# Optimization experiments

Measured on AMD Instinct MI355X. Metric: run time of the kernel, lower is better.

## Reference

```python
import jax, jax.numpy as jnp
import numpy as np

B, T, D, H, L, R, V = 4, 1024, 1024, 16, 12, 32, 50257
HD = D // H
SCALING = 2.0   # lora_alpha(64) / lora_rank(32) at the default 16-bit precision
EPS = 1e-5
KV_QMAX = float(2 ** 8 - 1)  # kv_cache_bits = 8 (middle of [4,8,16])


def _ln(x, g, b):
    m = jnp.mean(x, -1, keepdims=True)
    v = jnp.mean(jnp.square(x - m), -1, keepdims=True)
    return (x - m) * jax.lax.rsqrt(v + EPS) * g + b


def _round_ste(x):
    return x + jax.lax.stop_gradient(jnp.round(x) - x)


def _fake_quant(x, mn, mx):
    # asymmetric learnable fake-quant with straight-through rounding
    scale = (mx - mn) / KV_QMAX
    zp = _round_ste(-mn / scale)
    q = jnp.clip(_round_ste(x / scale) + zp, 0.0, KV_QMAX)
    return (q - zp) * scale


def _sp_linear(x, w, b, la, lb):
    # quantized-base linear (full precision at 16-bit) + LoRA adapter (eval: no dropout)
    return x @ w + b + SCALING * ((x @ la) @ lb)


def setup_inputs() -> dict:
    key = jax.random.key(0)
    ks = iter(jax.random.split(key, 64))
    rn = lambda shape, s=0.02: jax.random.normal(next(ks), shape, jnp.float32) * s
    return {
        "input_ids": jax.random.randint(next(ks), (B, T), 0, V),
        "wte": rn((V, D)), "wpe": rn((T, D)),
        "ln1_g": jnp.ones((L, D)), "ln1_b": jnp.zeros((L, D)),
        "attn_w": rn((L, D, 3 * D)), "attn_b": jnp.zeros((L, 3 * D)),
        "attn_la": rn((L, D, R)), "attn_lb": rn((L, R, 3 * D)),
        "proj_w": rn((L, D, D)), "proj_b": jnp.zeros((L, D)),
        "proj_la": rn((L, D, R)), "proj_lb": rn((L, R, D)),
        "ln2_g": jnp.ones((L, D)), "ln2_b": jnp.zeros((L, D)),
        "fc_w": rn((L, D, 4 * D)), "fc_b": jnp.zeros((L, 4 * D)),
        "fc_la": rn((L, D, R)), "fc_lb": rn((L, R, 4 * D)),
        "mproj_w": rn((L, 4 * D, D)), "mproj_b": jnp.zeros((L, D)),
        "mproj_la": rn((L, 4 * D, R)), "mproj_lb": rn((L, R, D)),
        "kv_min": jnp.full((L,), -4.0), "kv_max": jnp.full((L,), 4.0),
        "lnf_g": jnp.ones((D,)), "lnf_b": jnp.zeros((D,)),
    }


def reference(input_ids, wte, wpe, ln1_g, ln1_b, attn_w, attn_b, attn_la, attn_lb,
              proj_w, proj_b, proj_la, proj_lb, ln2_g, ln2_b, fc_w, fc_b, fc_la,
              fc_lb, mproj_w, mproj_b, mproj_la, mproj_lb, kv_min, kv_max,
              lnf_g, lnf_b):
    mask = jnp.tril(jnp.ones((T, T), bool))
    h = wte[input_ids] + wpe[None, :T]  # [B,T,D] (dropout is identity in eval)

    def block(h, p):
        (g1, b1, aw, ab, ala, alb, pw, pb, pla, plb, g2, b2,
         fw, fb, fla, flb, mw, mb, mla, mlb, mn, mx) = p
        x = _ln(h, g1, b1)
        qkv = _sp_linear(x, aw, ab, ala, alb)  # [B,T,3D]
        q, k, v = jnp.split(qkv, 3, axis=-1)
        heads = lambda t: t.reshape(B, T, H, HD).transpose(0, 2, 1, 3)  # bhtd
        q, k, v = heads(q), heads(k), heads(v)
        # KV-cache fake quantization (default precision flag unset on attn)
        k = _fake_quant(k, mn, mx)
        v = _fake_quant(v, mn, mx)
        att = jnp.einsum('bhqd,bhkd->bhqk', q, k) / np.float32(np.sqrt(HD))
        att = jax.nn.softmax(jnp.where(mask, att, -jnp.inf), axis=-1)
        o = jnp.einsum('bhqk,bhkd->bhqd', att, v).transpose(0, 2, 1, 3).reshape(B, T, D)
        h = h + _sp_linear(o, pw, pb, pla, plb)
        x = _ln(h, g2, b2)
        m = jax.nn.gelu(_sp_linear(x, fw, fb, fla, flb), approximate=False)
        h = h + _sp_linear(m, mw, mb, mla, mlb)
        return h, None

    params = (ln1_g, ln1_b, attn_w, attn_b, attn_la, attn_lb, proj_w, proj_b,
              proj_la, proj_lb, ln2_g, ln2_b, fc_w, fc_b, fc_la, fc_lb,
              mproj_w, mproj_b, mproj_la, mproj_lb, kv_min, kv_max)
    h, _ = jax.lax.scan(block, h, params)
    return _ln(h, lnf_g, lnf_b)
```

## Files before the change

### kernel.cpp

```cpp
#include <hip/hip_runtime.h>
#include <hip/hip_bf16.h>


typedef __bf16 bf16x8 __attribute__((ext_vector_type(8)));
typedef float f32x4 __attribute__((ext_vector_type(4)));

static __device__ __forceinline__ float bf2f(unsigned short u) {
    union { unsigned int i; float f; } c; c.i = ((unsigned int)u) << 16; return c.f;
}
static __device__ __forceinline__ unsigned short f2bf(float f) {
    unsigned int u = __float_as_uint(f);
    u += 0x7fffu + ((u >> 16) & 1u);
    return (unsigned short)(u >> 16);
}

#define GL2LDS(g, l) __builtin_amdgcn_global_load_lds( \
    (const __attribute__((address_space(1))) unsigned int*)(g), \
    (__attribute__((address_space(3))) unsigned int*)(l), 16, 0, 0)

__global__ __launch_bounds__(256) void k_embed(const int* __restrict__ ids,
        const float* __restrict__ wte, const float* __restrict__ wpe,
        float* __restrict__ h) {
    int row = blockIdx.x;
    int t = row & 1023;
    int id = ids[row];
    int d = threadIdx.x * 4;
    float4 a = *(const float4*)(wte + (size_t)id * 1024 + d);
    float4 b = *(const float4*)(wpe + (size_t)t * 1024 + d);
    float4 o = make_float4(a.x + b.x, a.y + b.y, a.z + b.z, a.w + b.w);
    *(float4*)(h + (size_t)row * 1024 + d) = o;
}

template <bool BF16OUT>
__global__ __launch_bounds__(256) void k_ln(const float* __restrict__ h,
        const float* __restrict__ g, const float* __restrict__ be,
        unsigned short* __restrict__ xo, float* __restrict__ fo) {
    int row = blockIdx.x, tid = threadIdx.x;
    float4 v = *(const float4*)(h + (size_t)row * 1024 + tid * 4);
    float s = v.x + v.y + v.z + v.w;
    for (int off = 32; off; off >>= 1) s += __shfl_down(s, off);
    __shared__ float red[8];
    int wid = tid >> 6, lane = tid & 63;
    if (!lane) red[wid] = s;
    __syncthreads();
    float mean = (red[0] + red[1] + red[2] + red[3]) * (1.f / 1024.f);
    float dx = v.x - mean, dy = v.y - mean, dz = v.z - mean, dw = v.w - mean;
    float q = dx * dx + dy * dy + dz * dz + dw * dw;
    for (int off = 32; off; off >>= 1) q += __shfl_down(q, off);
    if (!lane) red[4 + wid] = q;
    __syncthreads();
    float var = (red[4] + red[5] + red[6] + red[7]) * (1.f / 1024.f);
    float inv = 1.0f / sqrtf(var + 1e-5f);
    float4 gv = *(const float4*)(g + tid * 4);
    float4 bv = *(const float4*)(be + tid * 4);
    float y0 = dx * inv * gv.x + bv.x;
    float y1 = dy * inv * gv.y + bv.y;
    float y2 = dz * inv * gv.z + bv.z;
    float y3 = dw * inv * gv.w + bv.w;
    if (BF16OUT) {
        ushort4 o;
        o.x = f2bf(y0); o.y = f2bf(y1); o.z = f2bf(y2); o.w = f2bf(y3);
        *(ushort4*)(xo + (size_t)row * 1024 + tid * 4) = o;
    } else {
        *(float4*)(fo + (size_t)row * 1024 + tid * 4) = make_float4(y0, y1, y2, y3);
    }
}

__global__ __launch_bounds__(64) void k_lora_mfma(const unsigned short* __restrict__ A,
        const unsigned short* __restrict__ laT, unsigned short* __restrict__ tmp, int K) {
    int rowBase = blockIdx.x * 16;
    int lane = threadIdx.x;
    int lrow = lane & 15, lk8 = (lane >> 4) * 8;
    f32x4 acc0 = {0.f, 0.f, 0.f, 0.f}, acc1 = {0.f, 0.f, 0.f, 0.f};
    const unsigned short* arow = A + (size_t)(rowBase + lrow) * K + lk8;
    const unsigned short* b0p = laT + (size_t)lrow * K + lk8;
    const unsigned short* b1p = laT + (size_t)(16 + lrow) * K + lk8;
#pragma unroll 2
    for (int kt = 0; kt < K; kt += 32) {
        bf16x8 af = *(const bf16x8*)(arow + kt);
        bf16x8 b0 = *(const bf16x8*)(b0p + kt);
        bf16x8 b1 = *(const bf16x8*)(b1p + kt);
        acc0 = __builtin_amdgcn_mfma_f32_16x16x32_bf16(af, b0, acc0, 0, 0, 0);
        acc1 = __builtin_amdgcn_mfma_f32_16x16x32_bf16(af, b1, acc1, 0, 0, 0);
    }
    int lq = lane >> 4;
#pragma unroll
    for (int rg = 0; rg < 4; ++rg) {
        int row = rowBase + lq * 4 + rg;
        tmp[(size_t)row * 64 + lrow] = f2bf(acc0[rg]);
        tmp[(size_t)row * 64 + 16 + lrow] = f2bf(acc1[rg]);
        tmp[(size_t)row * 64 + 32 + lrow] = 0;
        tmp[(size_t)row * 64 + 48 + lrow] = 0;
    }
}

__global__ __launch_bounds__(256) void k_prep(
        const float* aw, const float* pw, const float* fw, const float* mw,
        const float* alb, const float* plb, const float* flb, const float* mlb,
        const float* ala, const float* pla, const float* fla, const float* mla,
        unsigned short* WTq, unsigned short* WTp, unsigned short* WTf, unsigned short* WTm,
        unsigned short* LTq, unsigned short* LTp, unsigned short* LTf, unsigned short* LTm,
        unsigned short* LAq, unsigned short* LAp, unsigned short* LAf, unsigned short* LAm) {
    int bid = blockIdx.x;
    const float* src; unsigned short* dst; int K, N, ntn, local, dstS; float scale = 1.f;
    if      (bid < 768)  { src = aw;  dst = WTq; K = 1024; N = 3072; ntn = 48; local = bid; dstS = K; }
    else if (bid < 1024) { src = pw;  dst = WTp; K = 1024; N = 1024; ntn = 16; local = bid - 768; dstS = K; }
    else if (bid < 2048) { src = fw;  dst = WTf; K = 1024; N = 4096; ntn = 64; local = bid - 1024; dstS = K; }
    else if (bid < 3072) { src = mw;  dst = WTm; K = 4096; N = 1024; ntn = 16; local = bid - 2048; dstS = K; }
    else if (bid < 3120) { src = alb; dst = LTq; K = 32;   N = 3072; ntn = 48; local = bid - 3072; scale = 2.f; dstS = 64; }
    else if (bid < 3136) { src = plb; dst = LTp; K = 32;   N = 1024; ntn = 16; local = bid - 3120; scale = 2.f; dstS = 64; }
    else if (bid < 3200) { src = flb; dst = LTf; K = 32;   N = 4096; ntn = 64; local = bid - 3136; scale = 2.f; dstS = 64; }
    else if (bid < 3216) { src = mlb; dst = LTm; K = 32;   N = 1024; ntn = 16; local = bid - 3200; scale = 2.f; dstS = 64; }
    else if (bid < 3232) { src = ala; dst = LAq; K = 1024; N = 32;   ntn = 1;  local = bid - 3216; dstS = K; }
    else if (bid < 3248) { src = pla; dst = LAp; K = 1024; N = 32;   ntn = 1;  local = bid - 3232; dstS = K; }
    else if (bid < 3264) { src = fla; dst = LAf; K = 1024; N = 32;   ntn = 1;  local = bid - 3248; dstS = K; }
    else                 { src = mla; dst = LAm; K = 4096; N = 32;   ntn = 1;  local = bid - 3264; dstS = K; }
    int kt = local / ntn, nt = local % ntn;
    int k0 = kt * 64, n0 = nt * 64;
    __shared__ unsigned short Tl[64][72];
    int tid = threadIdx.x;
    int cr = tid >> 6;
    int cc = tid & 63;
#pragma unroll
    for (int p = 0; p < 16; ++p) {
        int kl = p * 4 + cr;
        if (k0 + kl < K && n0 + cc < N) Tl[kl][cc] = f2bf(src[(size_t)(k0 + kl) * N + n0 + cc] * scale);
    }
    __syncthreads();
#pragma unroll
    for (int p = 0; p < 16; ++p) {
        int nl = p * 4 + cr;
        int kl = cc;
        if (n0 + nl < N) {
            if (k0 + kl < K) dst[(size_t)(n0 + nl) * dstS + k0 + kl] = Tl[kl][nl];
            else if (k0 + kl < dstS) dst[(size_t)(n0 + nl) * dstS + k0 + kl] = 0;
        }
    }
}

template <int EPI>
__global__ __launch_bounds__(256) void k_gemm(
        const unsigned short* __restrict__ A, const unsigned short* __restrict__ WT,
        const float* __restrict__ bias, const unsigned short* __restrict__ tmpA,
        const unsigned short* __restrict__ lbT, const float* __restrict__ res,
        float* __restrict__ outF, unsigned short* __restrict__ outH, int N, int K) {
    __shared__ unsigned short Al[128 * 32];
    __shared__ unsigned short Bl[128 * 32];
    int tid = threadIdx.x;
    int nBase = blockIdx.x * 128, rowBase = blockIdx.y * 128;
    int w = tid >> 6, lane = tid & 63;
    int wr = w >> 1, wc = w & 1;
    int lrow = lane & 15, lk8 = (lane >> 4) * 8;
    int srow = w * 32 + (lane >> 2);
    int scol = (lane & 3) * 8;
    f32x4 acc[4][4];
#pragma unroll
    for (int i = 0; i < 4; ++i)
#pragma unroll
        for (int j = 0; j < 4; ++j) acc[i][j] = f32x4{0.f, 0.f, 0.f, 0.f};
    int nk = K >> 5;
    for (int kt = 0; kt <= nk; ++kt) {
        bool mn = kt < nk;
        const unsigned short* sa0;
        const unsigned short* sa1;
        const unsigned short* sb0;
        const unsigned short* sb1;
        if (mn) {
            sa0 = A + (size_t)(rowBase + srow) * K + kt * 32 + scol;
            sa1 = A + (size_t)(rowBase + srow + 16) * K + kt * 32 + scol;
            sb0 = WT + (size_t)(nBase + srow) * K + kt * 32 + scol;
            sb1 = WT + (size_t)(nBase + srow + 16) * K + kt * 32 + scol;
        } else {
            sa0 = tmpA + (size_t)(rowBase + srow) * 64 + scol;
            sa1 = tmpA + (size_t)(rowBase + srow + 16) * 64 + scol;
            sb0 = lbT + (size_t)(nBase + srow) * 64 + scol;
            sb1 = lbT + (size_t)(nBase + srow + 16) * 64 + scol;
        }
        __syncthreads();
        GL2LDS(sa0, &Al[(w * 32) * 32]);
        GL2LDS(sa1, &Al[(w * 32 + 16) * 32]);
        GL2LDS(sb0, &Bl[(w * 32) * 32]);
        GL2LDS(sb1, &Bl[(w * 32 + 16) * 32]);
        __syncthreads();
        bf16x8 af[4], bfr[4];
#pragma unroll
        for (int mt = 0; mt < 4; ++mt) af[mt] = *(const bf16x8*)&Al[(wr * 64 + mt * 16 + lrow) * 32 + lk8];
#pragma unroll
        for (int nt = 0; nt < 4; ++nt) bfr[nt] = *(const bf16x8*)&Bl[(wc * 64 + nt * 16 + lrow) * 32 + lk8];
#pragma unroll
        for (int mt = 0; mt < 4; ++mt)
#pragma unroll
            for (int nt = 0; nt < 4; ++nt)
                acc[mt][nt] = __builtin_amdgcn_mfma_f32_16x16x32_bf16(af[mt], bfr[nt], acc[mt][nt], 0, 0, 0);
    }
    int lq = lane >> 4;
#pragma unroll
    for (int nt = 0; nt < 4; ++nt) {
        int col = nBase + wc * 64 + nt * 16 + lrow;
        float bv = bias[col];
#pragma unroll
        for (int mt = 0; mt < 4; ++mt) {
            int row0 = rowBase + wr * 64 + mt * 16 + lq * 4;
#pragma unroll
            for (int rg = 0; rg < 4; ++rg) {
                int row = row0 + rg;
                float v = acc[mt][nt][rg] + bv;
                size_t idx = (size_t)row * N + col;
                if (EPI == 1) v += res[idx];
                outF[idx] = v;
            }
        }
    }
}

template <int EPI>
__global__ __launch_bounds__(512, 1) void k_gemm256(
        const unsigned short* __restrict__ A, const unsigned short* __restrict__ WT,
        const float* __restrict__ bias, const unsigned short* __restrict__ tmpA,
        const unsigned short* __restrict__ lbT,
        const float* __restrict__ kvmin, const float* __restrict__ kvmax, int layer,
        unsigned short* __restrict__ qh, unsigned short* __restrict__ kh,
        unsigned short* __restrict__ vh,
        float* __restrict__ outF, unsigned short* __restrict__ outH, int N, int K) {
    __shared__ unsigned short lds[9 * 8192];
    const int tid = threadIdx.x;
    const int wid = tid >> 6, lane = tid & 63;
    const int wr = wid >> 2, wc = wid & 3;
    const int nBase = blockIdx.x * 256, rowBase = blockIdx.y * 256;
    const int nk = (K >> 6) + 1;

    f32x4 acc[8][4];
#pragma unroll
    for (int i = 0; i < 8; ++i)
#pragma unroll
        for (int j = 0; j < 4; ++j) acc[i][j] = f32x4{0.f, 0.f, 0.f, 0.f};

    auto stage = [&](int s) {
        int kt = s >> 2, part = s & 3;
        bool dead = kt >= nk;
        unsigned short* dst = &lds[(dead ? 8 : (s & 7)) * 8192];
        bool isA = part >= 2;
        int half = part & 1;
        bool lora = (kt == nk - 1);
#pragma unroll
        for (int i = 0; i < 2; ++i) {
            int o = ((i * 8 + wid) << 10) + (lane << 4);
            int r = o >> 7;
            int col = ((o & 127) ^ (((o >> 9) & 3) << 5)) >> 1;
            const unsigned short* src;
            if (dead) {
                src = A + (lane << 3);
            } else if (isA) {
                int grow = rowBase + half * 128 + r;
                src = lora ? tmpA + (size_t)grow * 64 + col
                           : A + (size_t)grow * K + kt * 64 + col;
            } else {
                int gcol = nBase + half * 128 + r;
                src = lora ? lbT + (size_t)gcol * 64 + col
                           : WT + (size_t)gcol * K + kt * 64 + col;
            }
            GL2LDS(src, dst + ((i * 8 + wid) << 9));
        }
    };

    stage(0); stage(1); stage(2); stage(3);
    stage(4); stage(5); stage(6);
    asm volatile("s_waitcnt vmcnt(6)" ::: "memory");
    __builtin_amdgcn_s_barrier();

    for (int kt = 0; kt < nk; ++kt) {
        const unsigned short* aPart = &lds[(((kt & 1) << 2) + 2 + wr) * 8192];
        const unsigned short* bPart = &lds[(((kt & 1) << 2) + (wc >> 1)) * 8192];
        bf16x8 bfr[4][2];
#pragma unroll
        for (int p = 0; p < 4; ++p) {
            bf16x8 af[2][2];
#pragma unroll
            for (int mm = 0; mm < 2; ++mm)
#pragma unroll
                for (int kk = 0; kk < 2; ++kk) {
                    int row = (p * 2 + mm) * 16 + (lane & 15);
                    int cb = (kk * 64 + ((lane >> 4) << 4)) ^ (((row >> 2) & 3) << 5);
                    af[mm][kk] = *(const bf16x8*)&aPart[row * 64 + (cb >> 1)];
                }
            if (p == 0) {
#pragma unroll
                for (int n = 0; n < 4; ++n)
#pragma unroll
                    for (int kk = 0; kk < 2; ++kk) {
                        int row = ((wc & 1) << 6) + n * 16 + (lane & 15);
                        int cb = (kk * 64 + ((lane >> 4) << 4)) ^ (((row >> 2) & 3) << 5);
                        bfr[n][kk] = *(const bf16x8*)&bPart[row * 64 + (cb >> 1)];
                    }
            }
            stage(p == 0 ? 4 * (kt + 1) + 3 : 4 * (kt + 2) + (p - 1));
            __builtin_amdgcn_s_barrier();
            __builtin_amdgcn_s_setprio(1);
#pragma unroll
            for (int mm = 0; mm < 2; ++mm)
#pragma unroll
                for (int n = 0; n < 4; ++n)
#pragma unroll
                    for (int kk = 0; kk < 2; ++kk)
                        acc[p * 2 + mm][n] = __builtin_amdgcn_mfma_f32_16x16x32_bf16(
                            af[mm][kk], bfr[n][kk], acc[p * 2 + mm][n], 0, 0, 0);
            __builtin_amdgcn_s_setprio(0);
            if (p == 3) asm volatile("s_waitcnt vmcnt(6)" ::: "memory");
            __builtin_amdgcn_s_barrier();
        }
    }

    if (EPI == 3) {
        const int b = rowBase >> 10, t0 = rowBase & 1023;
        const int sec = nBase >> 10, nb = nBase & 1023;
        const int lrow = lane & 15, lq4 = (lane >> 4) << 2;
        float qs = 1.f, qzp = 0.f, qinv = 1.f;
        if (sec) {
            float mnv = kvmin[layer], mxv = kvmax[layer];
            qs = (mxv - mnv) * (1.f / 255.f);
            qzp = rintf(-mnv / qs);
            qinv = 1.f / qs;
        }
#pragma unroll
        for (int n = 0; n < 4; ++n) {
            int dd = wc * 64 + n * 16 + lrow;
            float bv = bias[nBase + dd];
#pragma unroll
            for (int m = 0; m < 8; ++m) {
#pragma unroll
                for (int rg = 0; rg < 4; ++rg) {
                    int tt = wr * 128 + m * 16 + lq4 + rg;
                    float v = acc[m][n][rg] + bv;
                    if (sec) {
                        float qv = rintf(v * qinv) + qzp;
                        qv = fminf(fmaxf(qv, 0.f), 255.f);
                        v = (qv - qzp) * qs;
                    }
                    int r = (sec == 2) ? dd : tt;
                    int c = (sec == 2) ? tt : dd;
                    lds[r * 256 + (c ^ ((r & 7) << 3))] = f2bf(v);
                }
            }
        }
        __syncthreads();
        if (sec < 2) {
            unsigned short* dstp = sec ? kh : qh;
            int tL = tid & 255;
            int hp = tid >> 8;
#pragma unroll
            for (int hi = 0; hi < 2; ++hi) {
                int dL = (hp * 2 + hi) * 64;
                int hh = (nb >> 6) + hp * 2 + hi;
                size_t base = (((size_t)(b * 16 + hh)) * 1024 + t0 + tL) * 64;
#pragma unroll
                for (int j = 0; j < 8; ++j) {
                    int c = (dL + j * 8) ^ ((tL & 7) << 3);
                    *(uint4*)(dstp + base + j * 8) = *(const uint4*)&lds[tL * 256 + c];
                }
            }
        } else {
            int dL = tid & 255;
            int th = (tid >> 8) * 128;
            int hh = (nb >> 6) + (dL >> 6);
            size_t base = (((size_t)(b * 16 + hh)) * 64 + (dL & 63)) * 1024 + t0 + th;
#pragma unroll
            for (int j = 0; j < 16; ++j) {
                int c = (th + j * 8) ^ ((dL & 7) << 3);
                *(uint4*)(vh + base + j * 8) = *(const uint4*)&lds[dL * 256 + c];
            }
        }
    } else {
#pragma unroll
        for (int n = 0; n < 4; ++n) {
            int col = nBase + wc * 64 + n * 16 + (lane & 15);
            float bv = bias[col];
#pragma unroll
            for (int m = 0; m < 8; ++m) {
                int row0 = rowBase + wr * 128 + m * 16 + ((lane >> 4) << 2);
#pragma unroll
                for (int rg = 0; rg < 4; ++rg) {
                    int row = row0 + rg;
                    float v = acc[m][n][rg] + bv;
                    size_t idx = (size_t)row * N + col;
                    if (EPI == 2) {
                        v = 0.5f * v * (1.f + erff(v * 0.70710678118654752f));
                        outH[idx] = f2bf(v);
                    } else {
                        outF[idx] = v;
                    }
                }
            }
        }
    }
}

__global__ __launch_bounds__(256) void k_attn(const unsigned short* __restrict__ qh,
        const unsigned short* __restrict__ kh, const unsigned short* __restrict__ vh,
        unsigned short* __restrict__ o) {
    int fid = blockIdx.y * 16 + blockIdx.x;
    int wgid = (fid & 7) * 128 + (fid >> 3);
    int bh = wgid >> 4, qb = wgid & 15;
    int b = bh >> 4, hh = bh & 15;
    int tid = threadIdx.x, w = tid >> 6, lane = tid & 63;
    int cq = lane & 15;
    int g = lane >> 4;
    int lk8 = g * 8;
    __shared__ unsigned short Kl[64][72];
    __shared__ unsigned short Vt[64][72];
    __shared__ unsigned short Pl[4][16][72];
    const float SCL = 0.18033688011112042f;
    int qrow = qb * 64 + w * 16 + cq;
    bf16x8 aq[2];
    aq[0] = *(const bf16x8*)(qh + ((size_t)bh * 1024 + qrow) * 64 + lk8);
    aq[1] = *(const bf16x8*)(qh + ((size_t)bh * 1024 + qrow) * 64 + 32 + lk8);
    f32x4 od[4];
#pragma unroll
    for (int i = 0; i < 4; ++i) od[i] = f32x4{0.f, 0.f, 0.f, 0.f};
    float mrun = -3e38f, lrun = 0.f;
    int rl = tid >> 2, seg = (tid & 3) * 16;
    for (int kb = 0; kb <= qb; ++kb) {
        __syncthreads();
        {
            size_t kbase = ((size_t)bh * 1024 + kb * 64 + rl) * 64 + seg;
            *(uint4*)&Kl[rl][seg] = *(const uint4*)(kh + kbase);
            *(uint4*)&Kl[rl][seg + 8] = *(const uint4*)(kh + kbase + 8);
            size_t vbase = ((size_t)bh * 64 + rl) * 1024 + kb * 64 + seg;
            *(uint4*)&Vt[rl][seg] = *(const uint4*)(vh + vbase);
            *(uint4*)&Vt[rl][seg + 8] = *(const uint4*)(vh + vbase + 8);
        }
        __syncthreads();
        f32x4 st[4];
#pragma unroll
        for (int ktile = 0; ktile < 4; ++ktile) {
            f32x4 sacc = f32x4{0.f, 0.f, 0.f, 0.f};
#pragma unroll
            for (int dh = 0; dh < 2; ++dh) {
                bf16x8 bk = *(const bf16x8*)&Kl[ktile * 16 + cq][dh * 32 + lk8];
                sacc = __builtin_amdgcn_mfma_f32_16x16x32_bf16(bk, aq[dh], sacc, 0, 0, 0);
            }
            st[ktile] = sacc * SCL;
        }
        if (kb == qb) {
#pragma unroll
            for (int ktile = 0; ktile < 4; ++ktile) {
#pragma unroll
                for (int rg = 0; rg < 4; ++rg) {
                    int kidx = kb * 64 + ktile * 16 + g * 4 + rg;
                    if (kidx > qrow) st[ktile][rg] = -3e38f;
                }
            }
        }
        float pmax = st[0][0];
#pragma unroll
        for (int ktile = 0; ktile < 4; ++ktile)
#pragma unroll
            for (int rg = 0; rg < 4; ++rg) pmax = fmaxf(pmax, st[ktile][rg]);
        pmax = fmaxf(pmax, __shfl_xor(pmax, 16));
        pmax = fmaxf(pmax, __shfl_xor(pmax, 32));
        float mnew = fmaxf(mrun, pmax);
        float sum = 0.f;
#pragma unroll
        for (int ktile = 0; ktile < 4; ++ktile)
#pragma unroll
            for (int rg = 0; rg < 4; ++rg) {
                st[ktile][rg] = exp2f(st[ktile][rg] - mnew);
                sum += st[ktile][rg];
            }
        sum += __shfl_xor(sum, 16);
        sum += __shfl_xor(sum, 32);
        float corr = exp2f(mrun - mnew);
        lrun = lrun * corr + sum;
        mrun = mnew;
#pragma unroll
        for (int rg = 0; rg < 4; ++rg) {
            float cv = __shfl(corr, (lane & 48) | (g * 4 + rg));
#pragma unroll
            for (int dt = 0; dt < 4; ++dt) od[dt][rg] *= cv;
        }
#pragma unroll
        for (int ktile = 0; ktile < 4; ++ktile) {
            ushort4 pw;
            pw.x = f2bf(st[ktile][0]); pw.y = f2bf(st[ktile][1]);
            pw.z = f2bf(st[ktile][2]); pw.w = f2bf(st[ktile][3]);
            *(ushort4*)&Pl[w][cq][ktile * 16 + g * 4] = pw;
        }
        bf16x8 pa[2];
        pa[0] = *(const bf16x8*)&Pl[w][cq][lk8];
        pa[1] = *(const bf16x8*)&Pl[w][cq][32 + lk8];
#pragma unroll
        for (int dt = 0; dt < 4; ++dt) {
#pragma unroll
            for (int kh2 = 0; kh2 < 2; ++kh2) {
                bf16x8 bv = *(const bf16x8*)&Vt[dt * 16 + cq][kh2 * 32 + lk8];
                od[dt] = __builtin_amdgcn_mfma_f32_16x16x32_bf16(pa[kh2], bv, od[dt], 0, 0, 0);
            }
        }
    }
#pragma unroll
    for (int rg = 0; rg < 4; ++rg) {
        float lv = __shfl(lrun, (lane & 48) | (g * 4 + rg));
        float inv = 1.0f / lv;
        int row = qb * 64 + w * 16 + g * 4 + rg;
#pragma unroll
        for (int dt = 0; dt < 4; ++dt) {
            float val = od[dt][rg] * inv;
            o[((size_t)(b * 1024 + row)) * 1024 + hh * 64 + dt * 16 + cq] = f2bf(val);
        }
    }
}

extern "C" void kernel_launch(void* const* d_in, const int* in_sizes, int n_in,
                              void* d_out, int out_size, void* d_ws, size_t ws_size,
                              hipStream_t stream) {
    const int*   ids      = (const int*)d_in[0];
    const float* wte      = (const float*)d_in[1];
    const float* wpe      = (const float*)d_in[2];
    const float* ln1_g    = (const float*)d_in[3];
    const float* ln1_b    = (const float*)d_in[4];
    const float* attn_w   = (const float*)d_in[5];
    const float* attn_b   = (const float*)d_in[6];
    const float* attn_la  = (const float*)d_in[7];
    const float* attn_lb  = (const float*)d_in[8];
    const float* proj_w   = (const float*)d_in[9];
    const float* proj_b   = (const float*)d_in[10];
    const float* proj_la  = (const float*)d_in[11];
    const float* proj_lb  = (const float*)d_in[12];
    const float* ln2_g    = (const float*)d_in[13];
    const float* ln2_b    = (const float*)d_in[14];
    const float* fc_w     = (const float*)d_in[15];
    const float* fc_b     = (const float*)d_in[16];
    const float* fc_la    = (const float*)d_in[17];
    const float* fc_lb    = (const float*)d_in[18];
    const float* mproj_w  = (const float*)d_in[19];
    const float* mproj_b  = (const float*)d_in[20];
    const float* mproj_la = (const float*)d_in[21];
    const float* mproj_lb = (const float*)d_in[22];
    const float* kv_min   = (const float*)d_in[23];
    const float* kv_max   = (const float*)d_in[24];
    const float* lnf_g    = (const float*)d_in[25];
    const float* lnf_b    = (const float*)d_in[26];

    char* ws = (char*)d_ws;
    size_t off = 0;
    auto alloc = [&](size_t bytes) -> char* {
        char* p = ws + off;
        off = (off + bytes + 255) & ~(size_t)255;
        return p;
    };
    float*          h   = (float*)alloc(4096ull * 1024 * 4);
    unsigned short* xb  = (unsigned short*)alloc(4096ull * 1024 * 2);
    unsigned short* tmp = (unsigned short*)alloc(4096ull * 64 * 2);
    unsigned short* qhb = (unsigned short*)alloc(64ull * 1024 * 64 * 2);
    unsigned short* khb = (unsigned short*)alloc(64ull * 1024 * 64 * 2);
    unsigned short* vhb = (unsigned short*)alloc(64ull * 64 * 1024 * 2);
    unsigned short* ob  = (unsigned short*)alloc(4096ull * 1024 * 2);
    unsigned short* mb  = (unsigned short*)alloc(4096ull * 4096 * 2);
    unsigned short* WTq = (unsigned short*)alloc(3072ull * 1024 * 2);
    unsigned short* WTp = (unsigned short*)alloc(1024ull * 1024 * 2);
    unsigned short* WTf = (unsigned short*)alloc(4096ull * 1024 * 2);
    unsigned short* WTm = (unsigned short*)alloc(1024ull * 4096 * 2);
    unsigned short* LTq = (unsigned short*)alloc(3072ull * 64 * 2);
    unsigned short* LTp = (unsigned short*)alloc(1024ull * 64 * 2);
    unsigned short* LTf = (unsigned short*)alloc(4096ull * 64 * 2);
    unsigned short* LTm = (unsigned short*)alloc(1024ull * 64 * 2);
    unsigned short* LAq = (unsigned short*)alloc(32ull * 1024 * 2);
    unsigned short* LAp = (unsigned short*)alloc(32ull * 1024 * 2);
    unsigned short* LAf = (unsigned short*)alloc(32ull * 1024 * 2);
    unsigned short* LAm = (unsigned short*)alloc(32ull * 4096 * 2);

    k_embed<<<4096, 256, 0, stream>>>(ids, wte, wpe, h);
    for (int l = 0; l < 12; ++l) {
        k_prep<<<3328, 256, 0, stream>>>(
            attn_w + (size_t)l * 1024 * 3072, proj_w + (size_t)l * 1024 * 1024,
            fc_w + (size_t)l * 1024 * 4096, mproj_w + (size_t)l * 4096 * 1024,
            attn_lb + (size_t)l * 32 * 3072, proj_lb + (size_t)l * 32 * 1024,
            fc_lb + (size_t)l * 32 * 4096, mproj_lb + (size_t)l * 32 * 1024,
            attn_la + (size_t)l * 1024 * 32, proj_la + (size_t)l * 1024 * 32,
            fc_la + (size_t)l * 1024 * 32, mproj_la + (size_t)l * 4096 * 32,
            WTq, WTp, WTf, WTm, LTq, LTp, LTf, LTm, LAq, LAp, LAf, LAm);
        k_ln<true><<<4096, 256, 0, stream>>>(h, ln1_g + l * 1024, ln1_b + l * 1024, xb, nullptr);
        k_lora_mfma<<<256, 64, 0, stream>>>(xb, LAq, tmp, 1024);
        k_gemm256<3><<<dim3(12, 16), 512, 0, stream>>>(xb, WTq, attn_b + l * 3072, tmp, LTq,
                                                       kv_min, kv_max, l, qhb, khb, vhb,
                                                       nullptr, nullptr, 3072, 1024);
        k_attn<<<dim3(16, 64), 256, 0, stream>>>(qhb, khb, vhb, ob);
        k_lora_mfma<<<256, 64, 0, stream>>>(ob, LAp, tmp, 1024);
        k_gemm<1><<<dim3(8, 32), 256, 0, stream>>>(ob, WTp, proj_b + l * 1024, tmp, LTp,
                                                   h, h, nullptr, 1024, 1024);
        k_ln<true><<<4096, 256, 0, stream>>>(h, ln2_g + l * 1024, ln2_b + l * 1024, xb, nullptr);
        k_lora_mfma<<<256, 64, 0, stream>>>(xb, LAf, tmp, 1024);
        k_gemm256<2><<<dim3(16, 16), 512, 0, stream>>>(xb, WTf, fc_b + l * 4096, tmp, LTf,
                                                       nullptr, nullptr, 0, nullptr, nullptr, nullptr,
                                                       nullptr, mb, 4096, 1024);
        k_lora_mfma<<<256, 64, 0, stream>>>(mb, LAm, tmp, 4096);
        k_gemm<1><<<dim3(8, 32), 256, 0, stream>>>(mb, WTm, mproj_b + l * 1024, tmp, LTm,
                                                   h, h, nullptr, 1024, 4096);
    }
    k_ln<false><<<4096, 256, 0, stream>>>(h, lnf_g, lnf_b, nullptr, (float*)d_out);
}
```

Measured before the change: 4.419 ms.

## Split LoRA-A reduction across four waves and use 128x64 tiles for N=1024 GEMMs

The LoRA down-projection kernel now uses four waves per block. Each wave reduces a quarter of K, and the partial sums are combined through shared memory, so each block runs a quarter of the serial K loop. The proj and mproj GEMMs (N=1024) switch from 128x128 tiles with 4 waves to 128x64 tiles with 2 waves. This doubles the grid to 512 blocks for better CU occupancy on the wide GPU. The cost is more reloading of A tiles, less reuse per block, and an extra LDS reduction step.

```diff
diff --git a/kernel.cpp b/kernel.cpp
--- a/kernel.cpp
+++ b/kernel.cpp
@@ -66,31 +66,40 @@
     }
 }
 
-__global__ __launch_bounds__(64) void k_lora_mfma(const unsigned short* __restrict__ A,
+__global__ __launch_bounds__(256) void k_lora_mfma(const unsigned short* __restrict__ A,
         const unsigned short* __restrict__ laT, unsigned short* __restrict__ tmp, int K) {
     int rowBase = blockIdx.x * 16;
-    int lane = threadIdx.x;
+    int tid = threadIdx.x, w = tid >> 6, lane = tid & 63;
     int lrow = lane & 15, lk8 = (lane >> 4) * 8;
+    int kq = K >> 2;
     f32x4 acc0 = {0.f, 0.f, 0.f, 0.f}, acc1 = {0.f, 0.f, 0.f, 0.f};
-    const unsigned short* arow = A + (size_t)(rowBase + lrow) * K + lk8;
-    const unsigned short* b0p = laT + (size_t)lrow * K + lk8;
-    const unsigned short* b1p = laT + (size_t)(16 + lrow) * K + lk8;
+    const unsigned short* arow = A + (size_t)(rowBase + lrow) * K + w * kq + lk8;
+    const unsigned short* b0p = laT + (size_t)lrow * K + w * kq + lk8;
+    const unsigned short* b1p = laT + (size_t)(16 + lrow) * K + w * kq + lk8;
 #pragma unroll 2
-    for (int kt = 0; kt < K; kt += 32) {
+    for (int kt = 0; kt < kq; kt += 32) {
         bf16x8 af = *(const bf16x8*)(arow + kt);
         bf16x8 b0 = *(const bf16x8*)(b0p + kt);
         bf16x8 b1 = *(const bf16x8*)(b1p + kt);
         acc0 = __builtin_amdgcn_mfma_f32_16x16x32_bf16(af, b0, acc0, 0, 0, 0);
         acc1 = __builtin_amdgcn_mfma_f32_16x16x32_bf16(af, b1, acc1, 0, 0, 0);
     }
-    int lq = lane >> 4;
-#pragma unroll
-    for (int rg = 0; rg < 4; ++rg) {
-        int row = rowBase + lq * 4 + rg;
-        tmp[(size_t)row * 64 + lrow] = f2bf(acc0[rg]);
-        tmp[(size_t)row * 64 + 16 + lrow] = f2bf(acc1[rg]);
-        tmp[(size_t)row * 64 + 32 + lrow] = 0;
-        tmp[(size_t)row * 64 + 48 + lrow] = 0;
+    __shared__ f32x4 red[2][4][64];
+    red[0][w][lane] = acc0;
+    red[1][w][lane] = acc1;
+    __syncthreads();
+    if (w == 0) {
+        acc0 = red[0][0][lane] + red[0][1][lane] + red[0][2][lane] + red[0][3][lane];
+        acc1 = red[1][0][lane] + red[1][1][lane] + red[1][2][lane] + red[1][3][lane];
+        int lq = lane >> 4;
+#pragma unroll
+        for (int rg = 0; rg < 4; ++rg) {
+            int row = rowBase + lq * 4 + rg;
+            tmp[(size_t)row * 64 + lrow] = f2bf(acc0[rg]);
+            tmp[(size_t)row * 64 + 16 + lrow] = f2bf(acc1[rg]);
+            tmp[(size_t)row * 64 + 32 + lrow] = 0;
+            tmp[(size_t)row * 64 + 48 + lrow] = 0;
+        }
     }
 }
 
@@ -139,19 +148,18 @@
 }
 
 template <int EPI>
-__global__ __launch_bounds__(256) void k_gemm(
+__global__ __launch_bounds__(128) void k_gemm64(
         const unsigned short* __restrict__ A, const unsigned short* __restrict__ WT,
         const float* __restrict__ bias, const unsigned short* __restrict__ tmpA,
         const unsigned short* __restrict__ lbT, const float* __restrict__ res,
-        float* __restrict__ outF, unsigned short* __restrict__ outH, int N, int K) {
+        float* __restrict__ outF, int N, int K) {
     __shared__ unsigned short Al[128 * 32];
-    __shared__ unsigned short Bl[128 * 32];
+    __shared__ unsigned short Bl[64 * 32];
     int tid = threadIdx.x;
-    int nBase = blockIdx.x * 128, rowBase = blockIdx.y * 128;
+    int nBase = blockIdx.x * 64, rowBase = blockIdx.y * 128;
     int w = tid >> 6, lane = tid & 63;
-    int wr = w >> 1, wc = w & 1;
     int lrow = lane & 15, lk8 = (lane >> 4) * 8;
-    int srow = w * 32 + (lane >> 2);
+    int srow = lane >> 2;
     int scol = (lane & 3) * 8;
     f32x4 acc[4][4];
 #pragma unroll
@@ -161,32 +169,31 @@
     int nk = K >> 5;
     for (int kt = 0; kt <= nk; ++kt) {
         bool mn = kt < nk;
-        const unsigned short* sa0;
-        const unsigned short* sa1;
-        const unsigned short* sb0;
-        const unsigned short* sb1;
-        if (mn) {
-            sa0 = A + (size_t)(rowBase + srow) * K + kt * 32 + scol;
-            sa1 = A + (size_t)(rowBase + srow + 16) * K + kt * 32 + scol;
-            sb0 = WT + (size_t)(nBase + srow) * K + kt * 32 + scol;
-            sb1 = WT + (size_t)(nBase + srow + 16) * K + kt * 32 + scol;
-        } else {
-            sa0 = tmpA + (size_t)(rowBase + srow) * 64 + scol;
-            sa1 = tmpA + (size_t)(rowBase + srow + 16) * 64 + scol;
-            sb0 = lbT + (size_t)(nBase + srow) * 64 + scol;
-            sb1 = lbT + (size_t)(nBase + srow + 16) * 64 + scol;
+        const unsigned short* sa[4];
+        const unsigned short* sb[2];
+#pragma unroll
+        for (int i = 0; i < 4; ++i) {
+            int r = rowBase + w * 64 + i * 16 + srow;
+            sa[i] = mn ? A + (size_t)r * K + kt * 32 + scol
+                       : tmpA + (size_t)r * 64 + scol;
+        }
+#pragma unroll
+        for (int i = 0; i < 2; ++i) {
+            int r = nBase + w * 32 + i * 16 + srow;
+            sb[i] = mn ? WT + (size_t)r * K + kt * 32 + scol
+                       : lbT + (size_t)r * 64 + scol;
         }
         __syncthreads();
-        GL2LDS(sa0, &Al[(w * 32) * 32]);
-        GL2LDS(sa1, &Al[(w * 32 + 16) * 32]);
-        GL2LDS(sb0, &Bl[(w * 32) * 32]);
-        GL2LDS(sb1, &Bl[(w * 32 + 16) * 32]);
+#pragma unroll
+        for (int i = 0; i < 4; ++i) GL2LDS(sa[i], &Al[(w * 64 + i * 16) * 32]);
+#pragma unroll
+        for (int i = 0; i < 2; ++i) GL2LDS(sb[i], &Bl[(w * 32 + i * 16) * 32]);
         __syncthreads();
         bf16x8 af[4], bfr[4];
 #pragma unroll
-        for (int mt = 0; mt < 4; ++mt) af[mt] = *(const bf16x8*)&Al[(wr * 64 + mt * 16 + lrow) * 32 + lk8];
-#pragma unroll
-        for (int nt = 0; nt < 4; ++nt) bfr[nt] = *(const bf16x8*)&Bl[(wc * 64 + nt * 16 + lrow) * 32 + lk8];
+        for (int mt = 0; mt < 4; ++mt) af[mt] = *(const bf16x8*)&Al[(w * 64 + mt * 16 + lrow) * 32 + lk8];
+#pragma unroll
+        for (int nt = 0; nt < 4; ++nt) bfr[nt] = *(const bf16x8*)&Bl[(nt * 16 + lrow) * 32 + lk8];
 #pragma unroll
         for (int mt = 0; mt < 4; ++mt)
 #pragma unroll
@@ -196,11 +203,11 @@
     int lq = lane >> 4;
 #pragma unroll
     for (int nt = 0; nt < 4; ++nt) {
-        int col = nBase + wc * 64 + nt * 16 + lrow;
+        int col = nBase + nt * 16 + lrow;
         float bv = bias[col];
 #pragma unroll
         for (int mt = 0; mt < 4; ++mt) {
-            int row0 = rowBase + wr * 64 + mt * 16 + lq * 4;
+            int row0 = rowBase + w * 64 + mt * 16 + lq * 4;
 #pragma unroll
             for (int rg = 0; rg < 4; ++rg) {
                 int row = row0 + rg;
@@ -579,22 +586,22 @@
             fc_la + (size_t)l * 1024 * 32, mproj_la + (size_t)l * 4096 * 32,
             WTq, WTp, WTf, WTm, LTq, LTp, LTf, LTm, LAq, LAp, LAf, LAm);
         k_ln<true><<<4096, 256, 0, stream>>>(h, ln1_g + l * 1024, ln1_b + l * 1024, xb, nullptr);
-        k_lora_mfma<<<256, 64, 0, stream>>>(xb, LAq, tmp, 1024);
+        k_lora_mfma<<<256, 256, 0, stream>>>(xb, LAq, tmp, 1024);
         k_gemm256<3><<<dim3(12, 16), 512, 0, stream>>>(xb, WTq, attn_b + l * 3072, tmp, LTq,
                                                        kv_min, kv_max, l, qhb, khb, vhb,
                                                        nullptr, nullptr, 3072, 1024);
         k_attn<<<dim3(16, 64), 256, 0, stream>>>(qhb, khb, vhb, ob);
-        k_lora_mfma<<<256, 64, 0, stream>>>(ob, LAp, tmp, 1024);
-        k_gemm<1><<<dim3(8, 32), 256, 0, stream>>>(ob, WTp, proj_b + l * 1024, tmp, LTp,
-                                                   h, h, nullptr, 1024, 1024);
+        k_lora_mfma<<<256, 256, 0, stream>>>(ob, LAp, tmp, 1024);
+        k_gemm64<1><<<dim3(16, 32), 128, 0, stream>>>(ob, WTp, proj_b + l * 1024, tmp, LTp,
+                                                      h, h, 1024, 1024);
         k_ln<true><<<4096, 256, 0, stream>>>(h, ln2_g + l * 1024, ln2_b + l * 1024, xb, nullptr);
-        k_lora_mfma<<<256, 64, 0, stream>>>(xb, LAf, tmp, 1024);
+        k_lora_mfma<<<256, 256, 0, stream>>>(xb, LAf, tmp, 1024);
         k_gemm256<2><<<dim3(16, 16), 512, 0, stream>>>(xb, WTf, fc_b + l * 4096, tmp, LTf,
                                                        nullptr, nullptr, 0, nullptr, nullptr, nullptr,
                                                        nullptr, mb, 4096, 1024);
-        k_lora_mfma<<<256, 64, 0, stream>>>(mb, LAm, tmp, 4096);
-        k_gemm<1><<<dim3(8, 32), 256, 0, stream>>>(mb, WTm, mproj_b + l * 1024, tmp, LTm,
-                                                   h, h, nullptr, 1024, 4096);
+        k_lora_mfma<<<256, 256, 0, stream>>>(mb, LAm, tmp, 4096);
+        k_gemm64<1><<<dim3(16, 32), 128, 0, stream>>>(mb, WTm, mproj_b + l * 1024, tmp, LTm,
+                                                      h, h, 1024, 4096);
     }
     k_ln<false><<<4096, 256, 0, stream>>>(h, lnf_g, lnf_b, nullptr, (float*)d_out);
 }
```

New measurement: 4.265 ms. -3.5%, faster.
